# Kernel optimization log

Measured on AMD Instinct MI355X. Metric: run time of the kernel, lower is better.

## Reference

```python
import jax, jax.numpy as jnp
import numpy as np

N = 1_000_000          # total nodes (polyline points)
PTS_PER_CLUSTER = 20
C = N // PTS_PER_CLUSTER  # 50_000 clusters (polylines)
B = 32                 # graphs in batch
IN_F, HID, OUT_F, NUM_LAYERS = 16, 64, 128, 3
EPS_LN = 1e-5


def _mlp(x, w1, b1, g, be, w2, b2):
    # Linear -> LayerNorm -> ReLU -> Linear
    h = x @ w1 + b1
    mu = jnp.mean(h, axis=-1, keepdims=True)
    var = jnp.var(h, axis=-1, keepdims=True)
    h = (h - mu) * jax.lax.rsqrt(var + EPS_LN) * g + be
    h = jax.nn.relu(h)
    return h @ w2 + b2


def setup_inputs() -> dict:
    key = jax.random.key(0)
    ks = iter(jax.random.split(key, 64))

    def lin(k, fi, fo):
        s = 1.0 / np.sqrt(fi)
        return jax.random.uniform(k, (fi, fo), jnp.float32, -s, s)

    x = jax.random.normal(next(ks), (N, IN_F), jnp.float32)
    clusters = (jnp.arange(N) // PTS_PER_CLUSTER).astype(jnp.int64)  # sorted, each cluster has 20 pts
    batch = ((clusters * B) // C).astype(jnp.int64)                  # consistent graph ids

    inp = {"x": x, "clusters": clusters, "batch": batch}
    # pre MLP: IN_F -> HID -> HID
    inp.update(pre_w1=lin(next(ks), IN_F, HID), pre_b1=jnp.zeros((HID,), jnp.float32),
               pre_g=jnp.ones((HID,), jnp.float32), pre_be=jnp.zeros((HID,), jnp.float32),
               pre_w2=lin(next(ks), HID, HID), pre_b2=jnp.zeros((HID,), jnp.float32))
    # subgraph layers: HID -> HID -> HID//2 (concat with pooled -> HID)
    for i in range(NUM_LAYERS):
        inp[f"l{i}_w1"] = lin(next(ks), HID, HID)
        inp[f"l{i}_b1"] = jnp.zeros((HID,), jnp.float32)
        inp[f"l{i}_g"] = jnp.ones((HID,), jnp.float32)
        inp[f"l{i}_be"] = jnp.zeros((HID,), jnp.float32)
        inp[f"l{i}_w2"] = lin(next(ks), HID, HID // 2)
        inp[f"l{i}_b2"] = jnp.zeros((HID // 2,), jnp.float32)
    # output MLP: HID -> HID -> OUT_F
    inp.update(out_w1=lin(next(ks), HID, HID), out_b1=jnp.zeros((HID,), jnp.float32),
               out_g=jnp.ones((HID,), jnp.float32), out_be=jnp.zeros((HID,), jnp.float32),
               out_w2=lin(next(ks), HID, OUT_F), out_b2=jnp.zeros((OUT_F,), jnp.float32))
    return inp


def reference(x, clusters, batch,
              pre_w1, pre_b1, pre_g, pre_be, pre_w2, pre_b2,
              l0_w1, l0_b1, l0_g, l0_be, l0_w2, l0_b2,
              l1_w1, l1_b1, l1_g, l1_be, l1_w2, l1_b2,
              l2_w1, l2_b1, l2_g, l2_be, l2_w2, l2_b2,
              out_w1, out_b1, out_g, out_be, out_w2, out_b2):
    x = x.astype(jnp.float32)
    out = _mlp(x, pre_w1, pre_b1, pre_g, pre_be, pre_w2, pre_b2)  # [N, HID]
    layer_params = [(l0_w1, l0_b1, l0_g, l0_be, l0_w2, l0_b2),
                    (l1_w1, l1_b1, l1_g, l1_be, l1_w2, l1_b2),
                    (l2_w1, l2_b1, l2_g, l2_be, l2_w2, l2_b2)]
    for p in layer_params:
        h = _mlp(out, *p)                                          # [N, HID/2]
        pooled = jax.ops.segment_max(h, clusters, num_segments=C)  # [C, HID/2] scatter-max
        out = jnp.concatenate([h, pooled[clusters]], axis=-1)      # [N, HID]
    # max_pool_x: per-cluster feature max + per-cluster batch id
    out = jax.ops.segment_max(out, clusters, num_segments=C)       # [C, HID]
    batch_out = jax.ops.segment_max(batch, clusters, num_segments=C)
    out = _mlp(out, out_w1, out_b1, out_g, out_be, out_w2, out_b2)  # [C, OUT_F]
    norm = jnp.linalg.norm(out, ord=2, axis=-1, keepdims=True)
    out = out / jnp.maximum(norm, 1e-12)
    return out, batch_out
```

## Files before the change

### kernel.cpp

```cpp
#include <hip/hip_runtime.h>


#define ASTR 72

typedef short v8s __attribute__((ext_vector_type(8)));
typedef float v4f __attribute__((ext_vector_type(4)));

#define MFMA __builtin_amdgcn_mfma_f32_16x16x32_bf16

#define OFF_PW1 0
#define OFF_PW2 2048
#define OFF_LW1(L) (6144 + (L) * 6144)
#define OFF_LW2(L) (OFF_LW1(L) + 4096)
#define OFF_OW1 24576
#define OFF_OW2 28672

__device__ __forceinline__ short bfb(float v) {
  __bf16 b = (__bf16)v;
  return __builtin_bit_cast(short, b);
}

template <int CTRL>
__device__ __forceinline__ float dppadd(float x) {
  int xi = __builtin_bit_cast(int, x);
  int yi = __builtin_amdgcn_update_dpp(xi, xi, CTRL, 0xF, 0xF, false);
  return x + __builtin_bit_cast(float, yi);
}
__device__ __forceinline__ float sum16(float x) {
  x = dppadd<0xB1>(x);
  x = dppadd<0x4E>(x);
  x = dppadd<0x141>(x);
  x = dppadd<0x140>(x);
  return x;
}

__device__ __forceinline__ void ln_relu_write(short* A, int mtb, int col,
                                              int quad, v4f* acc,
                                              const float* gv, const float* bev) {
  float mu[4], sq[4], rs[4];
#pragma unroll
  for (int r = 0; r < 4; ++r) {
    mu[r] = acc[0][r] + acc[1][r] + acc[2][r] + acc[3][r];
    sq[r] = fmaf(acc[0][r], acc[0][r], fmaf(acc[1][r], acc[1][r],
            fmaf(acc[2][r], acc[2][r], acc[3][r] * acc[3][r])));
  }
#pragma unroll
  for (int r = 0; r < 4; ++r) { mu[r] = sum16(mu[r]); sq[r] = sum16(sq[r]); }
#pragma unroll
  for (int r = 0; r < 4; ++r) {
    float m_ = mu[r] * (1.0f / 64.0f);
    float v_ = sq[r] * (1.0f / 64.0f) - m_ * m_;
    mu[r] = m_;
    rs[r] = rsqrtf(v_ + 1e-5f);
  }
#pragma unroll
  for (int t = 0; t < 4; ++t) {
#pragma unroll
    for (int r = 0; r < 4; ++r) {
      float val = fmaf((acc[t][r] - mu[r]) * rs[r], gv[t], bev[t]);
      A[(mtb + quad * 4 + r) * ASTR + t * 16 + col] = bfb(fmaxf(val, 0.f));
    }
  }
}

template <int NT>
__device__ __forceinline__ void plain_write(short* A, int mtb, int col,
                                            int quad, v4f* acc) {
#pragma unroll
  for (int t = 0; t < NT; ++t)
#pragma unroll
    for (int r = 0; r < 4; ++r)
      A[(mtb + quad * 4 + r) * ASTR + t * 16 + col] = bfb(acc[t][r]);
}

__global__ void kT(const float* __restrict__ pw1, const float* __restrict__ pw2,
                   const float* __restrict__ w1a, const float* __restrict__ w2a,
                   const float* __restrict__ w1b, const float* __restrict__ w2b,
                   const float* __restrict__ w1c, const float* __restrict__ w2c,
                   const float* __restrict__ ow1, const float* __restrict__ ow2,
                   short* __restrict__ ws) {
  const float* W; int K, F, Kpad, off;
  switch (blockIdx.x) {
    case 0: W = pw1; K = 16; F = 64;  Kpad = 32; off = OFF_PW1; break;
    case 1: W = pw2; K = 64; F = 64;  Kpad = 64; off = OFF_PW2; break;
    case 2: W = w1a; K = 64; F = 64;  Kpad = 64; off = OFF_LW1(0); break;
    case 3: W = w2a; K = 64; F = 32;  Kpad = 64; off = OFF_LW2(0); break;
    case 4: W = w1b; K = 64; F = 64;  Kpad = 64; off = OFF_LW1(1); break;
    case 5: W = w2b; K = 64; F = 32;  Kpad = 64; off = OFF_LW2(1); break;
    case 6: W = w1c; K = 64; F = 64;  Kpad = 64; off = OFF_LW1(2); break;
    case 7: W = w2c; K = 64; F = 32;  Kpad = 64; off = OFF_LW2(2); break;
    case 8: W = ow1; K = 64; F = 64;  Kpad = 64; off = OFF_OW1; break;
    default: W = ow2; K = 64; F = 128; Kpad = 64; off = OFF_OW2; break;
  }
  const int total = F * (Kpad >> 3);
  for (int i = threadIdx.x; i < total; i += blockDim.x) {
    const int f = i % F;
    const int kq = i / F;
    v8s h;
#pragma unroll
    for (int j = 0; j < 8; ++j) {
      const int k = kq * 8 + j;
      h[j] = bfb((k < K) ? W[k * F + f] : 0.f);
    }
    *(v8s*)(ws + off + f * Kpad + kq * 8) = h;
  }
}

__global__ void __launch_bounds__(256, 3)
kF(const float* __restrict__ x, const int* __restrict__ batch,
   const short* __restrict__ wsW,
   const float* __restrict__ pb1, const float* __restrict__ pg,
   const float* __restrict__ pbe, const float* __restrict__ pb2,
   const float* __restrict__ b1a, const float* __restrict__ ga,
   const float* __restrict__ bea, const float* __restrict__ b2a,
   const float* __restrict__ b1b, const float* __restrict__ gb,
   const float* __restrict__ beb, const float* __restrict__ b2b,
   const float* __restrict__ b1c, const float* __restrict__ gc_,
   const float* __restrict__ bec, const float* __restrict__ b2c,
   const float* __restrict__ ob1, const float* __restrict__ og,
   const float* __restrict__ obe, const float* __restrict__ ob2,
   float* __restrict__ out, int C) {
  __shared__ __align__(16) short act[4 * 80 * ASTR];
  const int tid = threadIdx.x;
  const int lane = tid & 63;
  const int wave = tid >> 6;
  const int col = lane & 15;
  const int quad = lane >> 4;
  const int cbase = blockIdx.x * 16 + wave * 4;
  if (cbase >= C) return;
  const int nc = min(4, C - cbase);
  const int nrows = nc * 20;
  const int ntiles = (nrows + 15) >> 4;
  short* A = act + wave * 80 * ASTR;

  {
    const float4* x4 = (const float4*)x;
    const long nb = (long)cbase * 20;
    const short4 z = {0, 0, 0, 0};
    for (int i = lane; i < nrows * 4; i += 64) {
      const int row = i >> 2, e = i & 3;
      float4 v = x4[(nb + row) * 4 + e];
      short4 s = {bfb(v.x), bfb(v.y), bfb(v.z), bfb(v.w)};
      *(short4*)(A + row * ASTR + e * 4) = s;
      *(short4*)(A + row * ASTR + 16 + e * 4) = z;
    }
    if (nrows < ntiles * 16) {
      for (int i = lane; i < (ntiles * 16 - nrows) * 18; i += 64) {
        const int row = nrows + i / 18, e = i % 18;
        *(short4*)(A + row * ASTR + e * 4) = z;
      }
    }
  }

  {
    v8s B[4]; float bv[4], gv[4], bev[4];
#pragma unroll
    for (int t = 0; t < 4; ++t) {
      B[t] = *(const v8s*)(wsW + OFF_PW1 + (t * 16 + col) * 32 + quad * 8);
      bv[t] = pb1[t * 16 + col];
      gv[t] = pg[t * 16 + col];
      bev[t] = pbe[t * 16 + col];
    }
    for (int T = 0; T < ntiles; ++T) {
      const int mt0 = T * 16;
      const v8s a = *(const v8s*)(A + (mt0 + col) * ASTR + quad * 8);
      v4f acc[4];
#pragma unroll
      for (int t = 0; t < 4; ++t) {
        acc[t] = (v4f){bv[t], bv[t], bv[t], bv[t]};
        acc[t] = MFMA(a, B[t], acc[t], 0, 0, 0);
      }
      ln_relu_write(A, mt0, col, quad, acc, gv, bev);
    }
  }

  {
    v8s B[8]; float bv[4];
#pragma unroll
    for (int t = 0; t < 4; ++t) {
#pragma unroll
      for (int ks = 0; ks < 2; ++ks)
        B[t * 2 + ks] = *(const v8s*)(wsW + OFF_PW2 + (t * 16 + col) * 64 + ks * 32 + quad * 8);
      bv[t] = pb2[t * 16 + col];
    }
    for (int T = 0; T < ntiles; ++T) {
      const int mt0 = T * 16;
      const v8s a0 = *(const v8s*)(A + (mt0 + col) * ASTR + quad * 8);
      const v8s a1 = *(const v8s*)(A + (mt0 + col) * ASTR + 32 + quad * 8);
      v4f acc[4];
#pragma unroll
      for (int t = 0; t < 4; ++t) {
        acc[t] = (v4f){bv[t], bv[t], bv[t], bv[t]};
        acc[t] = MFMA(a0, B[t * 2], acc[t], 0, 0, 0);
        acc[t] = MFMA(a1, B[t * 2 + 1], acc[t], 0, 0, 0);
      }
      plain_write<4>(A, mt0, col, quad, acc);
    }
  }

  const float* B1p[3] = {b1a, b1b, b1c};
  const float* Gp[3]  = {ga, gb, gc_};
  const float* BEp[3] = {bea, beb, bec};
  const float* B2p[3] = {b2a, b2b, b2c};

  for (int L = 0; L < 3; ++L) {
    v8s B1[8], B2[4];
    float b1v[4], gv[4], bev[4], b2v[2];
    const short* w1 = wsW + OFF_LW1(L);
    const short* w2 = wsW + OFF_LW2(L);
#pragma unroll
    for (int t = 0; t < 4; ++t) {
#pragma unroll
      for (int ks = 0; ks < 2; ++ks)
        B1[t * 2 + ks] = *(const v8s*)(w1 + (t * 16 + col) * 64 + ks * 32 + quad * 8);
      b1v[t] = B1p[L][t * 16 + col];
      gv[t] = Gp[L][t * 16 + col];
      bev[t] = BEp[L][t * 16 + col];
    }
#pragma unroll
    for (int t = 0; t < 2; ++t) {
#pragma unroll
      for (int ks = 0; ks < 2; ++ks)
        B2[t * 2 + ks] = *(const v8s*)(w2 + (t * 16 + col) * 64 + ks * 32 + quad * 8);
      b2v[t] = B2p[L][t * 16 + col];
    }
    for (int T = 0; T < ntiles; ++T) {
      const int mt0 = T * 16;
      const v8s a0 = *(const v8s*)(A + (mt0 + col) * ASTR + quad * 8);
      const v8s a1 = *(const v8s*)(A + (mt0 + col) * ASTR + 32 + quad * 8);
      v4f acc[4];
#pragma unroll
      for (int t = 0; t < 4; ++t) {
        acc[t] = (v4f){b1v[t], b1v[t], b1v[t], b1v[t]};
        acc[t] = MFMA(a0, B1[t * 2], acc[t], 0, 0, 0);
        acc[t] = MFMA(a1, B1[t * 2 + 1], acc[t], 0, 0, 0);
      }
      ln_relu_write(A, mt0, col, quad, acc, gv, bev);
      const v8s c0 = *(const v8s*)(A + (mt0 + col) * ASTR + quad * 8);
      const v8s c1 = *(const v8s*)(A + (mt0 + col) * ASTR + 32 + quad * 8);
      v4f h[2];
#pragma unroll
      for (int t = 0; t < 2; ++t) {
        h[t] = (v4f){b2v[t], b2v[t], b2v[t], b2v[t]};
        h[t] = MFMA(c0, B2[t * 2], h[t], 0, 0, 0);
        h[t] = MFMA(c1, B2[t * 2 + 1], h[t], 0, 0, 0);
      }
      plain_write<2>(A, mt0, col, quad, h);
    }
    {
      const int cl = quad, jp = col;
      if (cl < nc) {
        const uint* AU = (const uint*)A;
        float m0 = -3.4e38f, m1 = -3.4e38f;
#pragma unroll
        for (int r = 0; r < 20; ++r) {
          const uint v = AU[(cl * 20 + r) * (ASTR / 2) + jp];
          m0 = fmaxf(m0, __builtin_bit_cast(float, v << 16));
          m1 = fmaxf(m1, __builtin_bit_cast(float, v & 0xFFFF0000u));
        }
        const uint pv = (uint)(unsigned short)bfb(m0) |
                        ((uint)(unsigned short)bfb(m1) << 16);
        uint* AW = (uint*)A;
        if (L < 2) {
#pragma unroll
          for (int r = 0; r < 20; ++r)
            AW[(cl * 20 + r) * (ASTR / 2) + 16 + jp] = pv;
        } else {
          AW[cl * (ASTR / 2) + jp] = pv;
          AW[cl * (ASTR / 2) + 16 + jp] = pv;
        }
      }
    }
  }

  {
    v8s B[8]; float bv[4], gv[4], bev[4];
#pragma unroll
    for (int t = 0; t < 4; ++t) {
#pragma unroll
      for (int ks = 0; ks < 2; ++ks)
        B[t * 2 + ks] = *(const v8s*)(wsW + OFF_OW1 + (t * 16 + col) * 64 + ks * 32 + quad * 8);
      bv[t] = ob1[t * 16 + col];
      gv[t] = og[t * 16 + col];
      bev[t] = obe[t * 16 + col];
    }
    const v8s a0 = *(const v8s*)(A + col * ASTR + quad * 8);
    const v8s a1 = *(const v8s*)(A + col * ASTR + 32 + quad * 8);
    v4f acc[4];
#pragma unroll
    for (int t = 0; t < 4; ++t) {
      acc[t] = (v4f){bv[t], bv[t], bv[t], bv[t]};
      acc[t] = MFMA(a0, B[t * 2], acc[t], 0, 0, 0);
      acc[t] = MFMA(a1, B[t * 2 + 1], acc[t], 0, 0, 0);
    }
    ln_relu_write(A, 0, col, quad, acc, gv, bev);
  }
  {
    v4f acc[8];
    const v8s a0 = *(const v8s*)(A + col * ASTR + quad * 8);
    const v8s a1 = *(const v8s*)(A + col * ASTR + 32 + quad * 8);
#pragma unroll
    for (int half = 0; half < 2; ++half) {
      v8s B[8];
#pragma unroll
      for (int t = 0; t < 4; ++t)
#pragma unroll
        for (int ks = 0; ks < 2; ++ks)
          B[t * 2 + ks] = *(const v8s*)(wsW + OFF_OW2 +
                            ((half * 4 + t) * 16 + col) * 64 + ks * 32 + quad * 8);
#pragma unroll
      for (int t = 0; t < 4; ++t) {
        const float bv = ob2[(half * 4 + t) * 16 + col];
        v4f a = (v4f){bv, bv, bv, bv};
        a = MFMA(a0, B[t * 2], a, 0, 0, 0);
        a = MFMA(a1, B[t * 2 + 1], a, 0, 0, 0);
        acc[half * 4 + t] = a;
      }
    }
    float inv[4];
#pragma unroll
    for (int r = 0; r < 4; ++r) {
      float s = 0.f;
#pragma unroll
      for (int t = 0; t < 8; ++t) s = fmaf(acc[t][r], acc[t][r], s);
      s = sum16(s);
      inv[r] = 1.0f / fmaxf(sqrtf(s), 1e-12f);
    }
    if (quad == 0) {
#pragma unroll
      for (int r = 0; r < 4; ++r) {
        if (r < nc) {
          const long gcl = cbase + r;
#pragma unroll
          for (int t = 0; t < 8; ++t)
            out[gcl * 128 + t * 16 + col] = acc[t][r] * inv[r];
          if (col == 0) out[(long)C * 128 + gcl] = (float)batch[gcl * 20];
        }
      }
    }
  }
}

extern "C" void kernel_launch(void* const* d_in, const int* in_sizes, int n_in,
                              void* d_out, int out_size, void* d_ws, size_t ws_size,
                              hipStream_t stream) {
  const float* x     = (const float*)d_in[0];
  const int*   batch = (const int*)d_in[2];
  const float* pw1 = (const float*)d_in[3];
  const float* pb1 = (const float*)d_in[4];
  const float* pg  = (const float*)d_in[5];
  const float* pbe = (const float*)d_in[6];
  const float* pw2 = (const float*)d_in[7];
  const float* pb2 = (const float*)d_in[8];
  const float* w1a = (const float*)d_in[9];
  const float* b1a = (const float*)d_in[10];
  const float* ga  = (const float*)d_in[11];
  const float* bea = (const float*)d_in[12];
  const float* w2a = (const float*)d_in[13];
  const float* b2a = (const float*)d_in[14];
  const float* w1b = (const float*)d_in[15];
  const float* b1b = (const float*)d_in[16];
  const float* gb  = (const float*)d_in[17];
  const float* beb = (const float*)d_in[18];
  const float* w2b = (const float*)d_in[19];
  const float* b2b = (const float*)d_in[20];
  const float* w1c = (const float*)d_in[21];
  const float* b1c = (const float*)d_in[22];
  const float* gc  = (const float*)d_in[23];
  const float* bec = (const float*)d_in[24];
  const float* w2c = (const float*)d_in[25];
  const float* b2c = (const float*)d_in[26];
  const float* ow1 = (const float*)d_in[27];
  const float* ob1 = (const float*)d_in[28];
  const float* og  = (const float*)d_in[29];
  const float* obe = (const float*)d_in[30];
  const float* ow2 = (const float*)d_in[31];
  const float* ob2 = (const float*)d_in[32];

  const int N = in_sizes[0] / 16;
  const int C = N / 20;
  short* ws16 = (short*)d_ws;
  float* out = (float*)d_out;

  hipLaunchKernelGGL(kT, dim3(10), dim3(256), 0, stream,
                     pw1, pw2, w1a, w2a, w1b, w2b, w1c, w2c, ow1, ow2, ws16);

  const int blocks = (C + 15) / 16;
  hipLaunchKernelGGL(kF, dim3(blocks), dim3(256), 0, stream,
                     x, batch, (const short*)ws16,
                     pb1, pg, pbe, pb2,
                     b1a, ga, bea, b2a,
                     b1b, gb, beb, b2b,
                     b1c, gc, bec, b2c,
                     ob1, og, obe, ob2,
                     out, C);
}
```

Baseline: 324.7 us.

## Transpose MFMA operands so each lane owns a row, vectorizing LDS writes

Swaps the MFMA operand order so the weights become the A operand and activations the B operand. The output tile is then transposed, and each lane holds four consecutive features of one row. LayerNorm statistics now reduce across lanes with two xor shuffles instead of four DPP steps per row. Activation writes back to LDS and the final output stores become short4/float4 vector stores instead of scalar ones, and bias/gamma/beta are loaded as vec4. This aims to cut LDS store instructions and reduction overhead in the per-tile epilogue. The trade-off is possible LDS bank conflicts from the new vector store pattern.

```diff
diff --git a/kernel.cpp b/kernel.cpp
--- a/kernel.cpp
+++ b/kernel.cpp
@@ -18,59 +18,6 @@
 __device__ __forceinline__ short bfb(float v) {
   __bf16 b = (__bf16)v;
   return __builtin_bit_cast(short, b);
-}
-
-template <int CTRL>
-__device__ __forceinline__ float dppadd(float x) {
-  int xi = __builtin_bit_cast(int, x);
-  int yi = __builtin_amdgcn_update_dpp(xi, xi, CTRL, 0xF, 0xF, false);
-  return x + __builtin_bit_cast(float, yi);
-}
-__device__ __forceinline__ float sum16(float x) {
-  x = dppadd<0xB1>(x);
-  x = dppadd<0x4E>(x);
-  x = dppadd<0x141>(x);
-  x = dppadd<0x140>(x);
-  return x;
-}
-
-__device__ __forceinline__ void ln_relu_write(short* A, int mtb, int col,
-                                              int quad, v4f* acc,
-                                              const float* gv, const float* bev) {
-  float mu[4], sq[4], rs[4];
-#pragma unroll
-  for (int r = 0; r < 4; ++r) {
-    mu[r] = acc[0][r] + acc[1][r] + acc[2][r] + acc[3][r];
-    sq[r] = fmaf(acc[0][r], acc[0][r], fmaf(acc[1][r], acc[1][r],
-            fmaf(acc[2][r], acc[2][r], acc[3][r] * acc[3][r])));
-  }
-#pragma unroll
-  for (int r = 0; r < 4; ++r) { mu[r] = sum16(mu[r]); sq[r] = sum16(sq[r]); }
-#pragma unroll
-  for (int r = 0; r < 4; ++r) {
-    float m_ = mu[r] * (1.0f / 64.0f);
-    float v_ = sq[r] * (1.0f / 64.0f) - m_ * m_;
-    mu[r] = m_;
-    rs[r] = rsqrtf(v_ + 1e-5f);
-  }
-#pragma unroll
-  for (int t = 0; t < 4; ++t) {
-#pragma unroll
-    for (int r = 0; r < 4; ++r) {
-      float val = fmaf((acc[t][r] - mu[r]) * rs[r], gv[t], bev[t]);
-      A[(mtb + quad * 4 + r) * ASTR + t * 16 + col] = bfb(fmaxf(val, 0.f));
-    }
-  }
-}
-
-template <int NT>
-__device__ __forceinline__ void plain_write(short* A, int mtb, int col,
-                                            int quad, v4f* acc) {
-#pragma unroll
-  for (int t = 0; t < NT; ++t)
-#pragma unroll
-    for (int r = 0; r < 4; ++r)
-      A[(mtb + quad * 4 + r) * ASTR + t * 16 + col] = bfb(acc[t][r]);
 }
 
 __global__ void kT(const float* __restrict__ pw1, const float* __restrict__ pw2,
@@ -103,6 +50,61 @@
       h[j] = bfb((k < K) ? W[k * F + f] : 0.f);
     }
     *(v8s*)(ws + off + f * Kpad + kq * 8) = h;
+  }
+}
+
+template <int NT, int KS>
+__device__ __forceinline__ void mmT(const short* A, int tb, const v8s* Wf,
+                                    const v4f* bias4, int col, int quad,
+                                    v4f* acc) {
+#pragma unroll
+  for (int t = 0; t < NT; ++t) acc[t] = bias4[t];
+#pragma unroll
+  for (int ks = 0; ks < KS; ++ks) {
+    const v8s b = *(const v8s*)(A + (tb + col) * ASTR + ks * 32 + quad * 8);
+#pragma unroll
+    for (int t = 0; t < NT; ++t)
+      acc[t] = MFMA(Wf[t * KS + ks], b, acc[t], 0, 0, 0);
+  }
+}
+
+__device__ __forceinline__ void lnT_write(short* Aw, int tb, int col, int quad,
+                                          v4f* acc, const v4f* g4,
+                                          const v4f* be4) {
+  float mu = 0.f, sq = 0.f;
+#pragma unroll
+  for (int t = 0; t < 4; ++t)
+#pragma unroll
+    for (int r = 0; r < 4; ++r) {
+      mu += acc[t][r];
+      sq = fmaf(acc[t][r], acc[t][r], sq);
+    }
+  mu += __shfl_xor(mu, 16); mu += __shfl_xor(mu, 32);
+  sq += __shfl_xor(sq, 16); sq += __shfl_xor(sq, 32);
+  mu *= (1.0f / 64.0f);
+  const float var = sq * (1.0f / 64.0f) - mu * mu;
+  const float rs = rsqrtf(var + 1e-5f);
+#pragma unroll
+  for (int t = 0; t < 4; ++t) {
+    short4 s;
+#pragma unroll
+    for (int r = 0; r < 4; ++r) {
+      float v = fmaf((acc[t][r] - mu) * rs, g4[t][r], be4[t][r]);
+      ((short*)&s)[r] = bfb(fmaxf(v, 0.f));
+    }
+    *(short4*)(Aw + (tb + col) * ASTR + t * 16 + quad * 4) = s;
+  }
+}
+
+template <int NT>
+__device__ __forceinline__ void plainT_write(short* Aw, int tb, int col,
+                                             int quad, v4f* acc) {
+#pragma unroll
+  for (int t = 0; t < NT; ++t) {
+    short4 s;
+#pragma unroll
+    for (int r = 0; r < 4; ++r) ((short*)&s)[r] = bfb(acc[t][r]);
+    *(short4*)(Aw + (tb + col) * ASTR + t * 16 + quad * 4) = s;
   }
 }
 
@@ -153,48 +155,34 @@
   }
 
   {
-    v8s B[4]; float bv[4], gv[4], bev[4];
+    v8s Wf[4]; v4f b4[4], g4[4], be4[4];
 #pragma unroll
     for (int t = 0; t < 4; ++t) {
-      B[t] = *(const v8s*)(wsW + OFF_PW1 + (t * 16 + col) * 32 + quad * 8);
-      bv[t] = pb1[t * 16 + col];
-      gv[t] = pg[t * 16 + col];
-      bev[t] = pbe[t * 16 + col];
+      Wf[t] = *(const v8s*)(wsW + OFF_PW1 + (t * 16 + col) * 32 + quad * 8);
+      b4[t]  = *(const v4f*)(pb1 + t * 16 + quad * 4);
+      g4[t]  = *(const v4f*)(pg  + t * 16 + quad * 4);
+      be4[t] = *(const v4f*)(pbe + t * 16 + quad * 4);
     }
     for (int T = 0; T < ntiles; ++T) {
-      const int mt0 = T * 16;
-      const v8s a = *(const v8s*)(A + (mt0 + col) * ASTR + quad * 8);
       v4f acc[4];
-#pragma unroll
-      for (int t = 0; t < 4; ++t) {
-        acc[t] = (v4f){bv[t], bv[t], bv[t], bv[t]};
-        acc[t] = MFMA(a, B[t], acc[t], 0, 0, 0);
-      }
-      ln_relu_write(A, mt0, col, quad, acc, gv, bev);
-    }
-  }
-
-  {
-    v8s B[8]; float bv[4];
+      mmT<4, 1>(A, T * 16, Wf, b4, col, quad, acc);
+      lnT_write(A, T * 16, col, quad, acc, g4, be4);
+    }
+  }
+
+  {
+    v8s Wf[8]; v4f b4[4];
 #pragma unroll
     for (int t = 0; t < 4; ++t) {
 #pragma unroll
       for (int ks = 0; ks < 2; ++ks)
-        B[t * 2 + ks] = *(const v8s*)(wsW + OFF_PW2 + (t * 16 + col) * 64 + ks * 32 + quad * 8);
-      bv[t] = pb2[t * 16 + col];
+        Wf[t * 2 + ks] = *(const v8s*)(wsW + OFF_PW2 + (t * 16 + col) * 64 + ks * 32 + quad * 8);
+      b4[t] = *(const v4f*)(pb2 + t * 16 + quad * 4);
     }
     for (int T = 0; T < ntiles; ++T) {
-      const int mt0 = T * 16;
-      const v8s a0 = *(const v8s*)(A + (mt0 + col) * ASTR + quad * 8);
-      const v8s a1 = *(const v8s*)(A + (mt0 + col) * ASTR + 32 + quad * 8);
       v4f acc[4];
-#pragma unroll
-      for (int t = 0; t < 4; ++t) {
-        acc[t] = (v4f){bv[t], bv[t], bv[t], bv[t]};
-        acc[t] = MFMA(a0, B[t * 2], acc[t], 0, 0, 0);
-        acc[t] = MFMA(a1, B[t * 2 + 1], acc[t], 0, 0, 0);
-      }
-      plain_write<4>(A, mt0, col, quad, acc);
+      mmT<4, 2>(A, T * 16, Wf, b4, col, quad, acc);
+      plainT_write<4>(A, T * 16, col, quad, acc);
     }
   }
 
@@ -204,48 +192,33 @@
   const float* B2p[3] = {b2a, b2b, b2c};
 
   for (int L = 0; L < 3; ++L) {
-    v8s B1[8], B2[4];
-    float b1v[4], gv[4], bev[4], b2v[2];
+    v8s W1f[8], W2f[4];
+    v4f b14[4], g4[4], be4[4], b24[2];
     const short* w1 = wsW + OFF_LW1(L);
     const short* w2 = wsW + OFF_LW2(L);
 #pragma unroll
     for (int t = 0; t < 4; ++t) {
 #pragma unroll
       for (int ks = 0; ks < 2; ++ks)
-        B1[t * 2 + ks] = *(const v8s*)(w1 + (t * 16 + col) * 64 + ks * 32 + quad * 8);
-      b1v[t] = B1p[L][t * 16 + col];
-      gv[t] = Gp[L][t * 16 + col];
-      bev[t] = BEp[L][t * 16 + col];
+        W1f[t * 2 + ks] = *(const v8s*)(w1 + (t * 16 + col) * 64 + ks * 32 + quad * 8);
+      b14[t] = *(const v4f*)(B1p[L] + t * 16 + quad * 4);
+      g4[t]  = *(const v4f*)(Gp[L]  + t * 16 + quad * 4);
+      be4[t] = *(const v4f*)(BEp[L] + t * 16 + quad * 4);
     }
 #pragma unroll
     for (int t = 0; t < 2; ++t) {
 #pragma unroll
       for (int ks = 0; ks < 2; ++ks)
-        B2[t * 2 + ks] = *(const v8s*)(w2 + (t * 16 + col) * 64 + ks * 32 + quad * 8);
-      b2v[t] = B2p[L][t * 16 + col];
+        W2f[t * 2 + ks] = *(const v8s*)(w2 + (t * 16 + col) * 64 + ks * 32 + quad * 8);
+      b24[t] = *(const v4f*)(B2p[L] + t * 16 + quad * 4);
     }
     for (int T = 0; T < ntiles; ++T) {
-      const int mt0 = T * 16;
-      const v8s a0 = *(const v8s*)(A + (mt0 + col) * ASTR + quad * 8);
-      const v8s a1 = *(const v8s*)(A + (mt0 + col) * ASTR + 32 + quad * 8);
       v4f acc[4];
-#pragma unroll
-      for (int t = 0; t < 4; ++t) {
-        acc[t] = (v4f){b1v[t], b1v[t], b1v[t], b1v[t]};
-        acc[t] = MFMA(a0, B1[t * 2], acc[t], 0, 0, 0);
-        acc[t] = MFMA(a1, B1[t * 2 + 1], acc[t], 0, 0, 0);
-      }
-      ln_relu_write(A, mt0, col, quad, acc, gv, bev);
-      const v8s c0 = *(const v8s*)(A + (mt0 + col) * ASTR + quad * 8);
-      const v8s c1 = *(const v8s*)(A + (mt0 + col) * ASTR + 32 + quad * 8);
+      mmT<4, 2>(A, T * 16, W1f, b14, col, quad, acc);
+      lnT_write(A, T * 16, col, quad, acc, g4, be4);
       v4f h[2];
-#pragma unroll
-      for (int t = 0; t < 2; ++t) {
-        h[t] = (v4f){b2v[t], b2v[t], b2v[t], b2v[t]};
-        h[t] = MFMA(c0, B2[t * 2], h[t], 0, 0, 0);
-        h[t] = MFMA(c1, B2[t * 2 + 1], h[t], 0, 0, 0);
-      }
-      plain_write<2>(A, mt0, col, quad, h);
+      mmT<2, 2>(A, T * 16, W2f, b24, col, quad, h);
+      plainT_write<2>(A, T * 16, col, quad, h);
     }
     {
       const int cl = quad, jp = col;
@@ -274,69 +247,57 @@
   }
 
   {
-    v8s B[8]; float bv[4], gv[4], bev[4];
+    v8s Wf[8]; v4f b4[4], g4[4], be4[4];
 #pragma unroll
     for (int t = 0; t < 4; ++t) {
 #pragma unroll
       for (int ks = 0; ks < 2; ++ks)
-        B[t * 2 + ks] = *(const v8s*)(wsW + OFF_OW1 + (t * 16 + col) * 64 + ks * 32 + quad * 8);
-      bv[t] = ob1[t * 16 + col];
-      gv[t] = og[t * 16 + col];
-      bev[t] = obe[t * 16 + col];
-    }
-    const v8s a0 = *(const v8s*)(A + col * ASTR + quad * 8);
-    const v8s a1 = *(const v8s*)(A + col * ASTR + 32 + quad * 8);
+        Wf[t * 2 + ks] = *(const v8s*)(wsW + OFF_OW1 + (t * 16 + col) * 64 + ks * 32 + quad * 8);
+      b4[t]  = *(const v4f*)(ob1 + t * 16 + quad * 4);
+      g4[t]  = *(const v4f*)(og  + t * 16 + quad * 4);
+      be4[t] = *(const v4f*)(obe + t * 16 + quad * 4);
+    }
     v4f acc[4];
-#pragma unroll
-    for (int t = 0; t < 4; ++t) {
-      acc[t] = (v4f){bv[t], bv[t], bv[t], bv[t]};
-      acc[t] = MFMA(a0, B[t * 2], acc[t], 0, 0, 0);
-      acc[t] = MFMA(a1, B[t * 2 + 1], acc[t], 0, 0, 0);
-    }
-    ln_relu_write(A, 0, col, quad, acc, gv, bev);
+    mmT<4, 2>(A, 0, Wf, b4, col, quad, acc);
+    lnT_write(A, 0, col, quad, acc, g4, be4);
   }
   {
     v4f acc[8];
-    const v8s a0 = *(const v8s*)(A + col * ASTR + quad * 8);
-    const v8s a1 = *(const v8s*)(A + col * ASTR + 32 + quad * 8);
+    const v8s bb0 = *(const v8s*)(A + col * ASTR + quad * 8);
+    const v8s bb1 = *(const v8s*)(A + col * ASTR + 32 + quad * 8);
 #pragma unroll
     for (int half = 0; half < 2; ++half) {
-      v8s B[8];
+      v8s Wf[8];
 #pragma unroll
       for (int t = 0; t < 4; ++t)
 #pragma unroll
         for (int ks = 0; ks < 2; ++ks)
-          B[t * 2 + ks] = *(const v8s*)(wsW + OFF_OW2 +
-                            ((half * 4 + t) * 16 + col) * 64 + ks * 32 + quad * 8);
+          Wf[t * 2 + ks] = *(const v8s*)(wsW + OFF_OW2 +
+                             ((half * 4 + t) * 16 + col) * 64 + ks * 32 + quad * 8);
 #pragma unroll
       for (int t = 0; t < 4; ++t) {
-        const float bv = ob2[(half * 4 + t) * 16 + col];
-        v4f a = (v4f){bv, bv, bv, bv};
-        a = MFMA(a0, B[t * 2], a, 0, 0, 0);
-        a = MFMA(a1, B[t * 2 + 1], a, 0, 0, 0);
+        v4f a = *(const v4f*)(ob2 + (half * 4 + t) * 16 + quad * 4);
+        a = MFMA(Wf[t * 2], bb0, a, 0, 0, 0);
+        a = MFMA(Wf[t * 2 + 1], bb1, a, 0, 0, 0);
         acc[half * 4 + t] = a;
       }
     }
-    float inv[4];
-#pragma unroll
-    for (int r = 0; r < 4; ++r) {
-      float s = 0.f;
-#pragma unroll
-      for (int t = 0; t < 8; ++t) s = fmaf(acc[t][r], acc[t][r], s);
-      s = sum16(s);
-      inv[r] = 1.0f / fmaxf(sqrtf(s), 1e-12f);
-    }
-    if (quad == 0) {
-#pragma unroll
-      for (int r = 0; r < 4; ++r) {
-        if (r < nc) {
-          const long gcl = cbase + r;
-#pragma unroll
-          for (int t = 0; t < 8; ++t)
-            out[gcl * 128 + t * 16 + col] = acc[t][r] * inv[r];
-          if (col == 0) out[(long)C * 128 + gcl] = (float)batch[gcl * 20];
-        }
+    float sq = 0.f;
+#pragma unroll
+    for (int t = 0; t < 8; ++t)
+#pragma unroll
+      for (int r = 0; r < 4; ++r) sq = fmaf(acc[t][r], acc[t][r], sq);
+    sq += __shfl_xor(sq, 16); sq += __shfl_xor(sq, 32);
+    const float inv = 1.0f / fmaxf(sqrtf(sq), 1e-12f);
+    if (col < nc) {
+      const long gcl = cbase + col;
+#pragma unroll
+      for (int t = 0; t < 8; ++t) {
+        float4 v = {acc[t][0] * inv, acc[t][1] * inv,
+                    acc[t][2] * inv, acc[t][3] * inv};
+        *(float4*)(out + gcl * 128 + t * 16 + quad * 4) = v;
       }
+      if (quad == 0) out[(long)C * 128 + gcl] = (float)batch[gcl * 20];
     }
   }
 }
```

Measured after the change: 308.1 us. -5.1%, faster.
